# Performance work log

Measured on AMD Instinct MI355X. Metric: run time of the kernel, lower is better.

The kernel has to match this reference:

```python
import jax, jax.numpy as jnp
import numpy as np

B, T, IN, H = 64, 128, 64, 256  # batch, seq_len, input_size, hidden_size
G = 4 * H                        # gate dim


def setup_inputs() -> dict:
    key = jax.random.key(0)
    ks = jax.random.split(key, 8)
    f32 = jnp.float32

    def p(k, shape, scale=0.05):
        return (jax.random.normal(k, shape, dtype=f32) * scale)

    # forget-gate bias initialized to 1.0 (slice [H:2H]) as in the torch module
    b_mu = jnp.zeros((G,), f32).at[H:2 * H].set(1.0)
    lv = lambda shape: jnp.full(shape, -3.0, f32)  # logvar init = -3.0

    return {
        "x": jax.random.normal(ks[0], (B, T, IN), dtype=f32),
        # layer 0
        "w_ih_mu0": p(ks[1], (G, IN)),
        "w_ih_lv0": lv((G, IN)),
        "w_hh_mu0": p(ks[2], (G, H)),
        "w_hh_lv0": lv((G, H)),
        "b_ih_mu0": b_mu,
        "b_ih_lv0": lv((G,)),
        "b_hh_mu0": jnp.zeros((G,), f32),
        "b_hh_lv0": lv((G,)),
        # layer 1 (input size = H since unidirectional)
        "w_ih_mu1": p(ks[3], (G, H)),
        "w_ih_lv1": lv((G, H)),
        "w_hh_mu1": p(ks[4], (G, H)),
        "w_hh_lv1": lv((G, H)),
        "b_ih_mu1": b_mu,
        "b_ih_lv1": lv((G,)),
        "b_hh_mu1": jnp.zeros((G,), f32),
        "b_hh_lv1": lv((G,)),
    }


def _sample(mu, logvar, k):
    # reparameterization: mu + exp(0.5*logvar) * eps, fresh eps every call (every timestep)
    return mu + jnp.exp(0.5 * logvar) * jax.random.normal(k, mu.shape, mu.dtype)


def _lstm_layer(x_seq, wih_mu, wih_lv, whh_mu, whh_lv,
                bih_mu, bih_lv, bhh_mu, bhh_lv, layer_key):
    # x_seq: (T, B, in) -> (hs (T,B,H), h_T (B,H), c_T (B,H))
    Tn, Bn = x_seq.shape[0], x_seq.shape[1]
    Hn = whh_mu.shape[1]
    keys = jax.random.split(layer_key, Tn)
    h0 = jnp.zeros((Bn, Hn), x_seq.dtype)
    c0 = jnp.zeros((Bn, Hn), x_seq.dtype)

    def step(carry, inp):
        h, c = carry
        x_t, k = inp
        k1, k2, k3, k4 = jax.random.split(k, 4)
        wih = _sample(wih_mu, wih_lv, k1)
        whh = _sample(whh_mu, whh_lv, k2)
        bih = _sample(bih_mu, bih_lv, k3)
        bhh = _sample(bhh_mu, bhh_lv, k4)
        gates = x_t @ wih.T + bih + h @ whh.T + bhh  # (B, 4H)
        i, f, g, o = jnp.split(gates, 4, axis=-1)
        c = jax.nn.sigmoid(f) * c + jax.nn.sigmoid(i) * jnp.tanh(g)
        h = jax.nn.sigmoid(o) * jnp.tanh(c)
        return (h, c), h

    (hT, cT), hs = jax.lax.scan(step, (h0, c0), (x_seq, keys))
    return hs, hT, cT


def reference(x,
              w_ih_mu0, w_ih_lv0, w_hh_mu0, w_hh_lv0,
              b_ih_mu0, b_ih_lv0, b_hh_mu0, b_hh_lv0,
              w_ih_mu1, w_ih_lv1, w_hh_mu1, w_hh_lv1,
              b_ih_mu1, b_ih_lv1, b_hh_mu1, b_hh_lv1):
    base = jax.random.key(42)
    x_seq = jnp.transpose(x, (1, 0, 2))  # batch_first -> (T, B, IN)
    hs0, h0T, c0T = _lstm_layer(x_seq, w_ih_mu0, w_ih_lv0, w_hh_mu0, w_hh_lv0,
                                b_ih_mu0, b_ih_lv0, b_hh_mu0, b_hh_lv0,
                                jax.random.fold_in(base, 0))
    hs1, h1T, c1T = _lstm_layer(hs0, w_ih_mu1, w_ih_lv1, w_hh_mu1, w_hh_lv1,
                                b_ih_mu1, b_ih_lv1, b_hh_mu1, b_hh_lv1,
                                jax.random.fold_in(base, 1))
    output = jnp.transpose(hs1, (1, 0, 2))  # (B, T, H)
    h_n = jnp.stack([h0T, h1T])  # (num_layers, B, H)
    c_n = jnp.stack([c0T, c1T])
    return output, h_n, c_n
```

## Files before the change

### kernel.cpp

```cpp
#include <hip/hip_runtime.h>
#include <stdint.h>


typedef unsigned int u32;
typedef float f32x4 __attribute__((ext_vector_type(4)));

#define Bn 64
#define Tn 128
#define INn 64
#define Hn 256
#define Gn 1024
#define BH (Bn * Hn)

#define OFF_ELV_WIH0 0
#define OFF_ELV_WHH0 65536
#define OFF_ELV_WIH1 327680
#define OFF_ELV_WHH1 589824
#define OFF_ELV_B    851968
#define OFF_H0       856064
#define OFF_H1       (OFF_H0 + 2 * BH)
#define OFF_KEYS     (OFF_H1 + 2 * BH)
#define OFF_SLOTS    (OFF_KEYS + 2 * Tn * 8)
#define WS_FLOATS    (OFF_SLOTS + 256 * 32)
#define STATE_FLOATS (OFF_KEYS - OFF_H0)
#define OUT_HN       (Bn * Tn * Hn)

struct KP { u32 a, b; };

__device__ __forceinline__ void st_coh(float* p, float v) {
  __hip_atomic_store(p, v, __ATOMIC_RELAXED, __HIP_MEMORY_SCOPE_AGENT);
}
__device__ __forceinline__ u32 ld_flag(const u32* p) {
  return __hip_atomic_load(p, __ATOMIC_RELAXED, __HIP_MEMORY_SCOPE_AGENT);
}
__device__ __forceinline__ void st_flag(u32* p, u32 v) {
  __hip_atomic_store(p, v, __ATOMIC_RELAXED, __HIP_MEMORY_SCOPE_AGENT);
}

__device__ __forceinline__ KP tf(u32 k0, u32 k1, u32 x0, u32 x1) {
  u32 ks2 = k0 ^ k1 ^ 0x1BD11BDAu;
  x0 += k0; x1 += k1;
#define TFR(r) { x0 += x1; x1 = (x1 << (r)) | (x1 >> (32 - (r))); x1 ^= x0; }
  TFR(13) TFR(15) TFR(26) TFR(6)
  x0 += k1;  x1 += ks2 + 1u;
  TFR(17) TFR(29) TFR(16) TFR(24)
  x0 += ks2; x1 += k0 + 2u;
  TFR(13) TFR(15) TFR(26) TFR(6)
  x0 += k0;  x1 += k1 + 3u;
  TFR(17) TFR(29) TFR(16) TFR(24)
  x0 += k1;  x1 += ks2 + 4u;
  TFR(13) TFR(15) TFR(26) TFR(6)
  x0 += ks2; x1 += k0 + 5u;
#undef TFR
  KP o; o.a = x0; o.b = x1; return o;
}

__device__ __forceinline__ float n01(u32 bits) {
  float f = __uint_as_float((bits >> 9) | 0x3f800000u) - 1.0f;
  float u = fmaxf(-0.99999994f, f * 2.0f - 0.99999994f);
  float w = -log1pf(-u * u);
  float p;
  if (w < 5.0f) {
    float z = w - 2.5f;
    p = 2.81022636e-08f;
    p = 3.43273939e-07f  + p * z;
    p = -3.5233877e-06f  + p * z;
    p = -4.39150654e-06f + p * z;
    p = 0.00021858087f   + p * z;
    p = -0.00125372503f  + p * z;
    p = -0.00417768164f  + p * z;
    p = 0.246640727f     + p * z;
    p = 1.50140941f      + p * z;
  } else {
    float z = sqrtf(w) - 3.0f;
    p = -0.000200214257f;
    p = 0.000100950558f  + p * z;
    p = 0.00134934322f   + p * z;
    p = -0.00367342844f  + p * z;
    p = 0.00573950773f   + p * z;
    p = -0.0076224613f   + p * z;
    p = 0.00943887047f   + p * z;
    p = 1.00167406f      + p * z;
    p = 2.83297682f      + p * z;
  }
  return 1.41421356237f * (p * u);
}

#define POOL_BYTES 51360
#define WBUF_OFF   0
#define INB_OFF    16512
#define BIAS_OFF   51328

template<int LAYER>
__device__ __forceinline__ void sample_weights(
    const float* __restrict__ wihmu, const float* __restrict__ whhmu,
    const float* __restrict__ bihmu, const float* __restrict__ bhhmu,
    const float* __restrict__ ws, float* __restrict__ wbuf,
    float* __restrict__ bias2, int ts, int j0, int tid)
{
  constexpr int Kin  = LAYER ? Hn : INn;
  constexpr int Ktot = Kin + Hn;
  if (ts >= Tn) return;
  const u32* kp = (const u32*)(ws + OFF_KEYS) + (LAYER * Tn + ts) * 8;
  const float* elv_ih  = ws + (LAYER ? OFF_ELV_WIH1 : OFF_ELV_WIH0);
  const float* elv_hh  = ws + (LAYER ? OFF_ELV_WHH1 : OFF_ELV_WHH0);
  const float* belv_ih = ws + OFF_ELV_B + LAYER * 2048;
  const float* belv_hh = belv_ih + 1024;

  const int k = tid;
  if (k < Ktot) {
    bool iswih = k < Kin;
    u32 ka = iswih ? kp[0] : kp[2], kb = iswih ? kp[1] : kp[3];
    const float* mup  = iswih ? wihmu  : whhmu;
    const float* elvp = iswih ? elv_ih : elv_hh;
    int kk = iswih ? k : k - Kin;
    int kstride = iswih ? Kin : Hn;
    #pragma unroll
    for (int gi = 0; gi < 8; ++gi) {
      int g = (gi & 3) * Hn + j0 + (gi >> 2);
      int i = g * kstride + kk;
      KP r = tf(ka, kb, 0u, (u32)i);
      wbuf[gi * 516 + k] = mup[i] + elvp[i] * n01(r.a ^ r.b);
    }
  }
  if (tid < 8) {
    int g = (tid & 3) * Hn + j0 + (tid >> 2);
    KP rb = tf(kp[4], kp[5], 0u, (u32)g);
    KP rh = tf(kp[6], kp[7], 0u, (u32)g);
    bias2[tid] = bihmu[g] + belv_ih[g] * n01(rb.a ^ rb.b)
               + bhhmu[g] + belv_hh[g] * n01(rh.a ^ rh.b);
  }
}

template<int LAYER>
__device__ void step_body(
    const float* x,
    float* ws, float* out, int t, char* pool,
    float& creg, u32* slots)
{
  constexpr int Kin  = LAYER ? Hn : INn;
  constexpr int Ktot = Kin + Hn;
  constexpr int nch  = Ktot / 64;
  const int tid = threadIdx.x;
  const int lb  = blockIdx.x & 127;
  const int j0  = lb * 2;
  const int ts  = LAYER ? (t - 1) : t;

  float* wbuf  = (float*)(pool + WBUF_OFF);
  float* inb   = (float*)(pool + INB_OFF);
  float* gpart = (float*)(pool + INB_OFF);
  float* bias2 = (float*)(pool + BIAS_OFF);

  const float* hprev = ws + (LAYER ? OFF_H1 : OFF_H0) + (ts & 1) * BH;
  const float* h0in  = ws + OFF_H0 + ((ts + 1) & 1) * BH;

  f32x4 pf0[2], pf1[2], pf2[2], pf3[2];
  auto issue = [&](int c, f32x4* pf) {
    #pragma unroll
    for (int m = 0; m < 2; ++m) {
      int f = tid + 512 * m, b = f >> 4, q4 = (f & 15) * 4;
      if (LAYER == 0) {
        if (c == 0) {
          const float* p = x + (b * Tn + ts) * INn + q4;
          asm volatile("global_load_dwordx4 %0, %1, off"
                       : "=v"(pf[m]) : "v"(p) : "memory");
        } else {
          const float* p = hprev + b * Hn + (c - 1) * 64 + q4;
          asm volatile("global_load_dwordx4 %0, %1, off sc1"
                       : "=v"(pf[m]) : "v"(p) : "memory");
        }
      } else {
        const float* p = (c < 4) ? (h0in + b * Hn + c * 64 + q4)
                                 : (hprev + b * Hn + (c - 4) * 64 + q4);
        asm volatile("global_load_dwordx4 %0, %1, off sc1"
                     : "=v"(pf[m]) : "v"(p) : "memory");
      }
    }
  };
  auto pfsel = [&](int c) -> f32x4* {
    switch (c & 3) {
      case 0: return pf0;
      case 1: return pf1;
      case 2: return pf2;
      default: return pf3;
    }
  };
  auto writeb = [&](int c, f32x4* pf) {
    #pragma unroll
    for (int m = 0; m < 2; ++m) {
      int f = tid + 512 * m, b = f >> 4, seg = f & 15;
      int col = 4 * (seg ^ ((b >> 3) & 7));
      *(f32x4*)&inb[(((c & 1) << 6) + b) * 68 + col] = pf[m];
    }
  };

  issue(0, pf0); issue(1, pf1); issue(2, pf2); issue(3, pf3);
  asm volatile("s_waitcnt vmcnt(6)" ::: "memory");
  __builtin_amdgcn_sched_barrier(0);
  writeb(0, pf0);
  __syncthreads();

  const int kq    = tid >> 5;
  const int bp    = (tid >> 2) & 7;
  const int rhalf = (tid >> 1) & 1;
  const int jj    = tid & 1;
  const int colq  = 4 * (kq ^ bp);

  float acc[4][4];
  #pragma unroll
  for (int r = 0; r < 4; ++r)
    acc[r][0] = acc[r][1] = acc[r][2] = acc[r][3] = 0.f;

  #pragma unroll
  for (int c = 0; c < nch; ++c) {
    if (c + 4 < nch) issue(c + 4, pfsel(c + 4));
    float4 w4[4];
    #pragma unroll
    for (int s = 0; s < 4; ++s)
      w4[s] = *(const float4*)&wbuf[(jj * 4 + s) * 516 + c * 64 + kq * 4];
    #pragma unroll
    for (int rr = 0; rr < 4; ++rr) {
      int b = bp * 8 + rhalf * 4 + rr;
      float4 in4 = *(const float4*)&inb[(((c & 1) << 6) + b) * 68 + colq];
      #pragma unroll
      for (int s = 0; s < 4; ++s)
        acc[rr][s] += in4.x * w4[s].x + in4.y * w4[s].y
                    + in4.z * w4[s].z + in4.w * w4[s].w;
    }
    if (c + 1 < nch) {
      constexpr int last = nch - 1;
      const int hi = (c + 4 < last) ? (c + 4) : last;
      const int rem = hi - (c + 1);
      if (rem >= 3)      asm volatile("s_waitcnt vmcnt(6)" ::: "memory");
      else if (rem == 2) asm volatile("s_waitcnt vmcnt(4)" ::: "memory");
      else if (rem == 1) asm volatile("s_waitcnt vmcnt(2)" ::: "memory");
      else               asm volatile("s_waitcnt vmcnt(0)" ::: "memory");
      __builtin_amdgcn_sched_barrier(0);
      writeb(c + 1, pfsel(c + 1));
    }
    __syncthreads();
  }

  if (LAYER == 0) {
    if (tid < 128) {
      while (ld_flag(slots + (128 + tid) * 32) < (u32)t)
        __builtin_amdgcn_s_sleep(1);
    }
    asm volatile("" ::: "memory");
  }

  #pragma unroll
  for (int rr = 0; rr < 4; ++rr) {
    int r = rhalf * 4 + rr;
    float4 v = {acc[rr][0], acc[rr][1], acc[rr][2], acc[rr][3]};
    int col4 = (bp * 16 + r * 2 + jj) ^ bp;
    *(float4*)&gpart[kq * 520 + col4 * 4] = v;
  }
  __syncthreads();

  if (tid < 128) {
    const int b = tid >> 1, j2 = tid & 1;
    const int rbp = b >> 3, rr = b & 7;
    const int col4 = (rbp * 16 + rr * 2 + j2) ^ rbp;
    float4 gq = {0.f, 0.f, 0.f, 0.f};
    #pragma unroll
    for (int q = 0; q < 16; ++q) {
      float4 p = *(const float4*)&gpart[q * 520 + col4 * 4];
      gq.x += p.x; gq.y += p.y; gq.z += p.z; gq.w += p.w;
    }
    const int j = j0 + j2;
    float gI = gq.x + bias2[j2 * 4 + 0];
    float gF = gq.y + bias2[j2 * 4 + 1];
    float gG = gq.z + bias2[j2 * 4 + 2];
    float gO = gq.w + bias2[j2 * 4 + 3];

    float cp = creg;
    float si = 1.f / (1.f + expf(-gI));
    float sf = 1.f / (1.f + expf(-gF));
    float so = 1.f / (1.f + expf(-gO));
    float cn = sf * cp + si * tanhf(gG);
    float hn = so * tanhf(cn);
    creg = cn;
    float* hnx = ws + (LAYER ? OFF_H1 : OFF_H0) + ((ts + 1) & 1) * BH;
    st_coh(hnx + b * Hn + j, hn);
    if (LAYER == 0) {
      if (ts == Tn - 1) {
        out[OUT_HN + b * Hn + j] = hn;
        out[OUT_HN + 2 * BH + b * Hn + j] = cn;
      }
    } else {
      out[b * (Tn * Hn) + ts * Hn + j] = hn;
      if (ts == Tn - 1) {
        out[OUT_HN + BH + b * Hn + j] = hn;
        out[OUT_HN + 3 * BH + b * Hn + j] = cn;
      }
    }
  }
}

__global__ __launch_bounds__(512) void bayes_lstm_persist(
    const float* __restrict__ x,
    const float* __restrict__ wihmu0, const float* __restrict__ whhmu0,
    const float* __restrict__ bihmu0, const float* __restrict__ bhhmu0,
    const float* __restrict__ wihmu1, const float* __restrict__ whhmu1,
    const float* __restrict__ bihmu1, const float* __restrict__ bhhmu1,
    float* __restrict__ ws, float* __restrict__ out)
{
  __shared__ __align__(16) char pool[POOL_BYTES];
  const int tid = threadIdx.x, bid = blockIdx.x;
  const int layer = bid >> 7, j0 = (bid & 127) * 2;
  float* wbuf  = (float*)(pool + WBUF_OFF);
  float* bias2 = (float*)(pool + BIAS_OFF);
  u32* slots = (u32*)(ws + OFF_SLOTS);
  float creg = 0.f;

  if (layer == 0)
    sample_weights<0>(wihmu0, whhmu0, bihmu0, bhhmu0, ws, wbuf, bias2, 0, j0, tid);
  __syncthreads();

  for (int t = 0; t <= Tn; ++t) {
    if (layer == 0) {
      if (t < Tn) step_body<0>(x, ws, out, t, pool, creg, slots);
    } else {
      if (t >= 1) step_body<1>(x, ws, out, t, pool, creg, slots);
    }
    if (t == Tn) break;

    __syncthreads();
    if (tid == 0) st_flag(slots + bid * 32, (u32)(t + 1));

    if (layer == 0)
      sample_weights<0>(wihmu0, whhmu0, bihmu0, bhhmu0, ws, wbuf, bias2,
                        t + 1, j0, tid);
    else
      sample_weights<1>(wihmu1, whhmu1, bihmu1, bhhmu1, ws, wbuf, bias2,
                        t, j0, tid);

    if (tid < 128) {
      if (layer == 0) {
        while (ld_flag(slots + tid * 32) < (u32)(t + 1))
          __builtin_amdgcn_s_sleep(1);
      } else {
        while (ld_flag(slots + (128 + tid) * 32) < (u32)(t + 1))
          __builtin_amdgcn_s_sleep(1);
        while (ld_flag(slots + tid * 32) < (u32)(t + 1))
          __builtin_amdgcn_s_sleep(1);
      }
    }
    asm volatile("" ::: "memory");
    __syncthreads();
  }
}

__global__ __launch_bounds__(256) void bayes_lstm_prologue(
    const float* __restrict__ wihlv0, const float* __restrict__ whhlv0,
    const float* __restrict__ bihlv0, const float* __restrict__ bhhlv0,
    const float* __restrict__ wihlv1, const float* __restrict__ whhlv1,
    const float* __restrict__ bihlv1, const float* __restrict__ bhhlv1,
    float* __restrict__ ws)
{
  const int gt = blockIdx.x * 256 + threadIdx.x;
  const int stride = gridDim.x * 256;
  for (int i = gt; i < 65536; i += stride)
    ws[OFF_ELV_WIH0 + i] = expf(0.5f * wihlv0[i]);
  for (int i = gt; i < 262144; i += stride) {
    ws[OFF_ELV_WHH0 + i] = expf(0.5f * whhlv0[i]);
    ws[OFF_ELV_WIH1 + i] = expf(0.5f * wihlv1[i]);
    ws[OFF_ELV_WHH1 + i] = expf(0.5f * whhlv1[i]);
  }
  for (int i = gt; i < 1024; i += stride) {
    ws[OFF_ELV_B + i]        = expf(0.5f * bihlv0[i]);
    ws[OFF_ELV_B + 1024 + i] = expf(0.5f * bhhlv0[i]);
    ws[OFF_ELV_B + 2048 + i] = expf(0.5f * bihlv1[i]);
    ws[OFF_ELV_B + 3072 + i] = expf(0.5f * bhhlv1[i]);
  }
  for (int i = gt; i < STATE_FLOATS; i += stride)
    st_coh(ws + OFF_H0 + i, 0.f);
  for (int i = gt; i < 256 * 32; i += stride)
    st_flag((u32*)(ws + OFF_SLOTS) + i, 0u);
  if (gt < 2 * Tn) {
    int l = gt >> 7, ts = gt & 127;
    KP lk  = tf(0u, 42u, 0u, (u32)l);
    KP kt  = tf(lk.a, lk.b, 0u, (u32)ts);
    KP kw  = tf(kt.a, kt.b, 0u, 0u);
    KP ku  = tf(kt.a, kt.b, 0u, 1u);
    KP kbi = tf(kt.a, kt.b, 0u, 2u);
    KP kbh = tf(kt.a, kt.b, 0u, 3u);
    u32* kp = (u32*)(ws + OFF_KEYS) + gt * 8;
    kp[0] = kw.a;  kp[1] = kw.b;  kp[2] = ku.a;  kp[3] = ku.b;
    kp[4] = kbi.a; kp[5] = kbi.b; kp[6] = kbh.a; kp[7] = kbh.b;
  }
}

extern "C" void kernel_launch(void* const* d_in, const int* in_sizes, int n_in,
                              void* d_out, int out_size, void* d_ws, size_t ws_size,
                              hipStream_t stream) {
  (void)in_sizes; (void)n_in; (void)out_size;
  if (ws_size < (size_t)WS_FLOATS * sizeof(float)) return;

  const float* x      = (const float*)d_in[0];
  const float* wihmu0 = (const float*)d_in[1];
  const float* wihlv0 = (const float*)d_in[2];
  const float* whhmu0 = (const float*)d_in[3];
  const float* whhlv0 = (const float*)d_in[4];
  const float* bihmu0 = (const float*)d_in[5];
  const float* bihlv0 = (const float*)d_in[6];
  const float* bhhmu0 = (const float*)d_in[7];
  const float* bhhlv0 = (const float*)d_in[8];
  const float* wihmu1 = (const float*)d_in[9];
  const float* wihlv1 = (const float*)d_in[10];
  const float* whhmu1 = (const float*)d_in[11];
  const float* whhlv1 = (const float*)d_in[12];
  const float* bihmu1 = (const float*)d_in[13];
  const float* bihlv1 = (const float*)d_in[14];
  const float* bhhmu1 = (const float*)d_in[15];
  const float* bhhlv1 = (const float*)d_in[16];
  float* ws  = (float*)d_ws;
  float* out = (float*)d_out;

  bayes_lstm_prologue<<<dim3(256), dim3(256), 0, stream>>>(
      wihlv0, whhlv0, bihlv0, bhhlv0, wihlv1, whhlv1, bihlv1, bhhlv1, ws);

  bayes_lstm_persist<<<dim3(256), dim3(512), 0, stream>>>(
      x, wihmu0, whhmu0, bihmu0, bhhmu0,
      wihmu1, whhmu1, bihmu1, bhhmu1, ws, out);
}
```

Before: 2.073 ms.

## Use atomic counter barriers and transposed hidden-state layout for recurrence

Replaces the per-block flag slots, which up to 128 threads polled, with two per-layer atomic counters that a single thread polls. It also stores hidden states transposed as [H][B], so each block writes contiguous batch entries for its two hidden units, and scatters the transposed data into the shared-memory input tile. The goal is less polling traffic on the inter-block barriers and more coalesced hidden-state stores. In exchange, all blocks now contend on the atomic counters and the shared-memory writes become scalar.

Result: slower. 2.163 ms (+4.4%).

```diff
diff --git a/kernel.cpp b/kernel.cpp
--- a/kernel.cpp
+++ b/kernel.cpp
@@ -17,12 +17,11 @@
 #define OFF_ELV_WIH1 327680
 #define OFF_ELV_WHH1 589824
 #define OFF_ELV_B    851968
-#define OFF_H0       856064
-#define OFF_H1       (OFF_H0 + 2 * BH)
-#define OFF_KEYS     (OFF_H1 + 2 * BH)
-#define OFF_SLOTS    (OFF_KEYS + 2 * Tn * 8)
-#define WS_FLOATS    (OFF_SLOTS + 256 * 32)
-#define STATE_FLOATS (OFF_KEYS - OFF_H0)
+#define OFF_H0T      856064
+#define OFF_H1T      (OFF_H0T + 2 * Hn * Bn)
+#define OFF_KEYS     (OFF_H1T + 2 * Hn * Bn)
+#define OFF_BAR      (OFF_KEYS + 2 * Tn * 8)
+#define WS_FLOATS    (OFF_BAR + 64)
 #define OUT_HN       (Bn * Tn * Hn)
 
 struct KP { u32 a, b; };
@@ -136,14 +135,13 @@
 __device__ void step_body(
     const float* x,
     float* ws, float* out, int t, char* pool,
-    float& creg, u32* slots)
+    float& creg, u32* bar)
 {
   constexpr int Kin  = LAYER ? Hn : INn;
   constexpr int Ktot = Kin + Hn;
   constexpr int nch  = Ktot / 64;
   const int tid = threadIdx.x;
-  const int lb  = blockIdx.x & 127;
-  const int j0  = lb * 2;
+  const int j0  = (blockIdx.x & 127) * 2;
   const int ts  = LAYER ? (t - 1) : t;
 
   float* wbuf  = (float*)(pool + WBUF_OFF);
@@ -151,27 +149,25 @@
   float* gpart = (float*)(pool + INB_OFF);
   float* bias2 = (float*)(pool + BIAS_OFF);
 
-  const float* hprev = ws + (LAYER ? OFF_H1 : OFF_H0) + (ts & 1) * BH;
-  const float* h0in  = ws + OFF_H0 + ((ts + 1) & 1) * BH;
+  const float* hT_self = ws + (LAYER ? OFF_H1T : OFF_H0T) + (ts & 1) * (Hn * Bn);
+  const float* hT_in   = ws + OFF_H0T + ((ts + 1) & 1) * (Hn * Bn);
 
   f32x4 pf0[2], pf1[2], pf2[2], pf3[2];
   auto issue = [&](int c, f32x4* pf) {
     #pragma unroll
     for (int m = 0; m < 2; ++m) {
-      int f = tid + 512 * m, b = f >> 4, q4 = (f & 15) * 4;
-      if (LAYER == 0) {
-        if (c == 0) {
-          const float* p = x + (b * Tn + ts) * INn + q4;
-          asm volatile("global_load_dwordx4 %0, %1, off"
-                       : "=v"(pf[m]) : "v"(p) : "memory");
-        } else {
-          const float* p = hprev + b * Hn + (c - 1) * 64 + q4;
-          asm volatile("global_load_dwordx4 %0, %1, off sc1"
-                       : "=v"(pf[m]) : "v"(p) : "memory");
-        }
+      int f = tid + 512 * m;
+      if (LAYER == 0 && c == 0) {
+        int b = f >> 4, q4 = (f & 15) * 4;
+        const float* p = x + (b * Tn + ts) * INn + q4;
+        asm volatile("global_load_dwordx4 %0, %1, off"
+                     : "=v"(pf[m]) : "v"(p) : "memory");
       } else {
-        const float* p = (c < 4) ? (h0in + b * Hn + c * 64 + q4)
-                                 : (hprev + b * Hn + (c - 4) * 64 + q4);
+        int k = f >> 4, b0 = (f & 15) * 4;
+        const float* p;
+        if (LAYER == 0)      p = hT_self + (c * 64 + k - 64) * Bn + b0;
+        else if (c < 4)      p = hT_in   + (c * 64 + k) * Bn + b0;
+        else                 p = hT_self + (c * 64 + k - 256) * Bn + b0;
         asm volatile("global_load_dwordx4 %0, %1, off sc1"
                      : "=v"(pf[m]) : "v"(p) : "memory");
       }
@@ -188,9 +184,21 @@
   auto writeb = [&](int c, f32x4* pf) {
     #pragma unroll
     for (int m = 0; m < 2; ++m) {
-      int f = tid + 512 * m, b = f >> 4, seg = f & 15;
-      int col = 4 * (seg ^ ((b >> 3) & 7));
-      *(f32x4*)&inb[(((c & 1) << 6) + b) * 68 + col] = pf[m];
+      int f = tid + 512 * m;
+      if (LAYER == 0 && c == 0) {
+        int b = f >> 4, seg = f & 15;
+        int col = 4 * (seg ^ ((b >> 3) & 7));
+        *(f32x4*)&inb[(((c & 1) << 6) + b) * 68 + col] = pf[m];
+      } else {
+        int k = f >> 4, b0 = (f & 15) * 4;
+        int q = k >> 2, kr = k & 3;
+        int base = (c & 1) << 6;
+        #pragma unroll
+        for (int i = 0; i < 4; ++i) {
+          int b = b0 + i;
+          inb[(base + b) * 68 + 4 * (q ^ ((b >> 3) & 7)) + kr] = pf[m][i];
+        }
+      }
     }
   };
 
@@ -242,9 +250,9 @@
   }
 
   if (LAYER == 0) {
-    if (tid < 128) {
-      while (ld_flag(slots + (128 + tid) * 32) < (u32)t)
-        __builtin_amdgcn_s_sleep(1);
+    if (tid == 0) {
+      while (ld_flag(bar + 32) < (u32)(128 * t))
+        __builtin_amdgcn_s_sleep(2);
     }
     asm volatile("" ::: "memory");
   }
@@ -281,8 +289,8 @@
     float cn = sf * cp + si * tanhf(gG);
     float hn = so * tanhf(cn);
     creg = cn;
-    float* hnx = ws + (LAYER ? OFF_H1 : OFF_H0) + ((ts + 1) & 1) * BH;
-    st_coh(hnx + b * Hn + j, hn);
+    float* hTn = ws + (LAYER ? OFF_H1T : OFF_H0T) + ((ts + 1) & 1) * (Hn * Bn);
+    st_coh(hTn + j * Bn + b, hn);
     if (LAYER == 0) {
       if (ts == Tn - 1) {
         out[OUT_HN + b * Hn + j] = hn;
@@ -311,7 +319,8 @@
   const int layer = bid >> 7, j0 = (bid & 127) * 2;
   float* wbuf  = (float*)(pool + WBUF_OFF);
   float* bias2 = (float*)(pool + BIAS_OFF);
-  u32* slots = (u32*)(ws + OFF_SLOTS);
+  u32* bar = (u32*)(ws + OFF_BAR);
+  u32* cnt_mine = bar + (bid >> 7) * 32;
   float creg = 0.f;
 
   if (layer == 0)
@@ -320,14 +329,16 @@
 
   for (int t = 0; t <= Tn; ++t) {
     if (layer == 0) {
-      if (t < Tn) step_body<0>(x, ws, out, t, pool, creg, slots);
+      if (t < Tn) step_body<0>(x, ws, out, t, pool, creg, bar);
     } else {
-      if (t >= 1) step_body<1>(x, ws, out, t, pool, creg, slots);
+      if (t >= 1) step_body<1>(x, ws, out, t, pool, creg, bar);
     }
     if (t == Tn) break;
 
     __syncthreads();
-    if (tid == 0) st_flag(slots + bid * 32, (u32)(t + 1));
+    if (tid == 0)
+      __hip_atomic_fetch_add(cnt_mine, 1u, __ATOMIC_RELAXED,
+                             __HIP_MEMORY_SCOPE_AGENT);
 
     if (layer == 0)
       sample_weights<0>(wihmu0, whhmu0, bihmu0, bhhmu0, ws, wbuf, bias2,
@@ -336,15 +347,13 @@
       sample_weights<1>(wihmu1, whhmu1, bihmu1, bhhmu1, ws, wbuf, bias2,
                         t, j0, tid);
 
-    if (tid < 128) {
-      if (layer == 0) {
-        while (ld_flag(slots + tid * 32) < (u32)(t + 1))
-          __builtin_amdgcn_s_sleep(1);
-      } else {
-        while (ld_flag(slots + (128 + tid) * 32) < (u32)(t + 1))
-          __builtin_amdgcn_s_sleep(1);
-        while (ld_flag(slots + tid * 32) < (u32)(t + 1))
-          __builtin_amdgcn_s_sleep(1);
+    if (tid == 0) {
+      const u32 tgt = (u32)(128 * (t + 1));
+      while (ld_flag(cnt_mine) < tgt)
+        __builtin_amdgcn_s_sleep(2);
+      if (layer == 1) {
+        while (ld_flag(bar) < tgt)
+          __builtin_amdgcn_s_sleep(2);
       }
     }
     asm volatile("" ::: "memory");
@@ -374,10 +383,10 @@
     ws[OFF_ELV_B + 2048 + i] = expf(0.5f * bihlv1[i]);
     ws[OFF_ELV_B + 3072 + i] = expf(0.5f * bhhlv1[i]);
   }
-  for (int i = gt; i < STATE_FLOATS; i += stride)
-    st_coh(ws + OFF_H0 + i, 0.f);
-  for (int i = gt; i < 256 * 32; i += stride)
-    st_flag((u32*)(ws + OFF_SLOTS) + i, 0u);
+  for (int i = gt; i < 4 * Hn * Bn; i += stride)
+    st_coh(ws + OFF_H0T + i, 0.f);
+  if (gt < 64)
+    st_flag((u32*)(ws + OFF_BAR) + gt, 0u);
   if (gt < 2 * Tn) {
     int l = gt >> 7, ts = gt & 127;
     KP lk  = tf(0u, 42u, 0u, (u32)l);
```

## Decouple LSTM layers with 4-deep layer-0 hidden ring and per-layer flags

Applied to the files above, without the earlier changes.

The layer-0 hidden-state buffer becomes a 4-slot ring instead of double buffering. Layer 1 now waits only on its own previous step and on layer 0 having produced the current step, instead of both layers advancing in lockstep each iteration. This lets layer 0 run up to a few steps ahead, removing the global two-layer barrier from the critical path. Layer-1 weight sampling moves into the prologue and the step index is realigned. It adds workspace and more complex flag dependencies, with a risk of ordering mistakes.

Measured after the change: 2.181 ms. 1.05x slower.

```diff
diff --git a/kernel.cpp b/kernel.cpp
--- a/kernel.cpp
+++ b/kernel.cpp
@@ -9,7 +9,6 @@
 #define Tn 128
 #define INn 64
 #define Hn 256
-#define Gn 1024
 #define BH (Bn * Hn)
 
 #define OFF_ELV_WIH0 0
@@ -18,7 +17,7 @@
 #define OFF_ELV_WHH1 589824
 #define OFF_ELV_B    851968
 #define OFF_H0       856064
-#define OFF_H1       (OFF_H0 + 2 * BH)
+#define OFF_H1       (OFF_H0 + 4 * BH)
 #define OFF_KEYS     (OFF_H1 + 2 * BH)
 #define OFF_SLOTS    (OFF_KEYS + 2 * Tn * 8)
 #define WS_FLOATS    (OFF_SLOTS + 256 * 32)
@@ -135,24 +134,24 @@
 template<int LAYER>
 __device__ void step_body(
     const float* x,
-    float* ws, float* out, int t, char* pool,
+    float* ws, float* out, int ts, char* pool,
     float& creg, u32* slots)
 {
   constexpr int Kin  = LAYER ? Hn : INn;
   constexpr int Ktot = Kin + Hn;
   constexpr int nch  = Ktot / 64;
   const int tid = threadIdx.x;
-  const int lb  = blockIdx.x & 127;
-  const int j0  = lb * 2;
-  const int ts  = LAYER ? (t - 1) : t;
+  const int j0  = (blockIdx.x & 127) * 2;
 
   float* wbuf  = (float*)(pool + WBUF_OFF);
   float* inb   = (float*)(pool + INB_OFF);
   float* gpart = (float*)(pool + INB_OFF);
   float* bias2 = (float*)(pool + BIAS_OFF);
 
-  const float* hprev = ws + (LAYER ? OFF_H1 : OFF_H0) + (ts & 1) * BH;
-  const float* h0in  = ws + OFF_H0 + ((ts + 1) & 1) * BH;
+  const float* hprev = LAYER
+      ? ws + OFF_H1 + ((ts + 1) & 1) * BH
+      : ws + OFF_H0 + ((ts + 3) & 3) * BH;
+  const float* h0in  = ws + OFF_H0 + (ts & 3) * BH;
 
   f32x4 pf0[2], pf1[2], pf2[2], pf3[2];
   auto issue = [&](int c, f32x4* pf) {
@@ -241,9 +240,9 @@
     __syncthreads();
   }
 
-  if (LAYER == 0) {
+  if (LAYER == 0 && ts >= 4) {
     if (tid < 128) {
-      while (ld_flag(slots + (128 + tid) * 32) < (u32)t)
+      while (ld_flag(slots + (128 + tid) * 32) < (u32)(ts - 3))
         __builtin_amdgcn_s_sleep(1);
     }
     asm volatile("" ::: "memory");
@@ -281,7 +280,8 @@
     float cn = sf * cp + si * tanhf(gG);
     float hn = so * tanhf(cn);
     creg = cn;
-    float* hnx = ws + (LAYER ? OFF_H1 : OFF_H0) + ((ts + 1) & 1) * BH;
+    float* hnx = LAYER ? ws + OFF_H1 + (ts & 1) * BH
+                       : ws + OFF_H0 + (ts & 3) * BH;
     st_coh(hnx + b * Hn + j, hn);
     if (LAYER == 0) {
       if (ts == Tn - 1) {
@@ -316,39 +316,41 @@
 
   if (layer == 0)
     sample_weights<0>(wihmu0, whhmu0, bihmu0, bhhmu0, ws, wbuf, bias2, 0, j0, tid);
+  else
+    sample_weights<1>(wihmu1, whhmu1, bihmu1, bhhmu1, ws, wbuf, bias2, 0, j0, tid);
   __syncthreads();
 
-  for (int t = 0; t <= Tn; ++t) {
-    if (layer == 0) {
-      if (t < Tn) step_body<0>(x, ws, out, t, pool, creg, slots);
-    } else {
-      if (t >= 1) step_body<1>(x, ws, out, t, pool, creg, slots);
-    }
-    if (t == Tn) break;
-
+  for (int ts = 0; ts < Tn; ++ts) {
+    if (tid < 128) {
+      if (layer == 0) {
+        if (ts >= 1) {
+          while (ld_flag(slots + tid * 32) < (u32)ts)
+            __builtin_amdgcn_s_sleep(1);
+        }
+      } else {
+        if (ts >= 1) {
+          while (ld_flag(slots + (128 + tid) * 32) < (u32)ts)
+            __builtin_amdgcn_s_sleep(1);
+        }
+        while (ld_flag(slots + tid * 32) < (u32)(ts + 1))
+          __builtin_amdgcn_s_sleep(1);
+      }
+    }
+    asm volatile("" ::: "memory");
     __syncthreads();
-    if (tid == 0) st_flag(slots + bid * 32, (u32)(t + 1));
+
+    if (layer == 0) step_body<0>(x, ws, out, ts, pool, creg, slots);
+    else            step_body<1>(x, ws, out, ts, pool, creg, slots);
+
+    __syncthreads();
+    if (tid == 0) st_flag(slots + bid * 32, (u32)(ts + 1));
 
     if (layer == 0)
       sample_weights<0>(wihmu0, whhmu0, bihmu0, bhhmu0, ws, wbuf, bias2,
-                        t + 1, j0, tid);
+                        ts + 1, j0, tid);
     else
       sample_weights<1>(wihmu1, whhmu1, bihmu1, bhhmu1, ws, wbuf, bias2,
-                        t, j0, tid);
-
-    if (tid < 128) {
-      if (layer == 0) {
-        while (ld_flag(slots + tid * 32) < (u32)(t + 1))
-          __builtin_amdgcn_s_sleep(1);
-      } else {
-        while (ld_flag(slots + (128 + tid) * 32) < (u32)(t + 1))
-          __builtin_amdgcn_s_sleep(1);
-        while (ld_flag(slots + tid * 32) < (u32)(t + 1))
-          __builtin_amdgcn_s_sleep(1);
-      }
-    }
-    asm volatile("" ::: "memory");
-    __syncthreads();
+                        ts + 1, j0, tid);
   }
 }
 
```
